# Performance work log

Hardware: AMD Instinct MI355X
Metric: run time of the kernel (lower is better)

Reference implementation:

```python
import jax, jax.numpy as jnp
import numpy as np

B, NN, S = 8, 511, 512          # graphs, nodes, seq (= nodes + graph token)
D, H, DH = 768, 12, 64          # hidden, heads, head dim
FFN, L = 3072, 6                # ffn size, layers
VOCAB = 512

def layer_norm(x, s, b, eps=1e-5):
    m = x.mean(-1, keepdims=True)
    v = ((x - m) ** 2).mean(-1, keepdims=True)
    return (x - m) / jnp.sqrt(v + eps) * s + b

def setup_inputs() -> dict:
    key = jax.random.key(0)
    ks = jax.random.split(key, 24)
    std = 0.02 / np.sqrt(L)
    inp = {}
    inp['attn_bias'] = jax.random.normal(ks[0], (B, S, S), jnp.float32) * 0.1
    inp['spatial_pos'] = jax.random.normal(ks[1], (B, NN, NN, 1), jnp.float32)
    inp['x'] = jax.random.randint(ks[2], (B, NN, 1), 0, VOCAB)
    node_emb = jax.random.normal(ks[3], (VOCAB, D), jnp.float32) * 0.02
    inp['node_emb'] = node_emb.at[0].set(0.0)  # padding_idx=0
    inp['graph_token'] = jax.random.normal(ks[4], (1, D), jnp.float32) * 0.02
    inp['virt_dist'] = jax.random.normal(ks[5], (1, H), jnp.float32) * 0.02
    inp['sp_w1'] = jax.random.normal(ks[6], (1, 128), jnp.float32) * std
    inp['sp_b1'] = jnp.zeros((128,), jnp.float32)
    inp['sp_w2'] = jax.random.normal(ks[7], (128, H), jnp.float32) * std
    inp['sp_b2'] = jnp.zeros((H,), jnp.float32)
    inp['ln1_s'] = jnp.ones((L, D), jnp.float32)
    inp['ln1_b'] = jnp.zeros((L, D), jnp.float32)
    inp['wq'] = jax.random.normal(ks[8], (L, D, D), jnp.float32) * std
    inp['bq'] = jnp.zeros((L, D), jnp.float32)
    inp['wk'] = jax.random.normal(ks[9], (L, D, D), jnp.float32) * std
    inp['bk'] = jnp.zeros((L, D), jnp.float32)
    inp['wv'] = jax.random.normal(ks[10], (L, D, D), jnp.float32) * std
    inp['bv'] = jnp.zeros((L, D), jnp.float32)
    inp['wo'] = jax.random.normal(ks[11], (L, D, D), jnp.float32) * std
    inp['bo'] = jnp.zeros((L, D), jnp.float32)
    inp['ln2_s'] = jnp.ones((L, D), jnp.float32)
    inp['ln2_b'] = jnp.zeros((L, D), jnp.float32)
    inp['fw1'] = jax.random.normal(ks[12], (L, D, FFN), jnp.float32) * std
    inp['fb1'] = jnp.zeros((L, FFN), jnp.float32)
    inp['fw2'] = jax.random.normal(ks[13], (L, FFN, D), jnp.float32) * std
    inp['fb2'] = jnp.zeros((L, D), jnp.float32)
    inp['fln_s'] = jnp.ones((D,), jnp.float32)
    inp['fln_b'] = jnp.zeros((D,), jnp.float32)
    return inp

def reference(attn_bias, spatial_pos, x, node_emb, graph_token, virt_dist,
              sp_w1, sp_b1, sp_w2, sp_b2,
              ln1_s, ln1_b, wq, bq, wk, bk, wv, bv, wo, bo,
              ln2_s, ln2_b, fw1, fb1, fw2, fb2, fln_s, fln_b):
    scale = DH ** -0.5
    # node features: embedding lookup summed over per-node feature indices
    h = node_emb[x].sum(axis=-2)                                   # [B, NN, D]
    h = jnp.concatenate([jnp.broadcast_to(graph_token[None], (B, 1, D)), h], axis=1)  # [B, S, D]
    # structural bias: spatial-pos MLP -> per-head bias on node block
    sp_bias = (spatial_pos @ sp_w1 + sp_b1) @ sp_w2 + sp_b2        # [B, NN, NN, H]
    sp_bias = sp_bias.transpose(0, 3, 1, 2)                         # [B, H, NN, NN]
    # original adds attn_bias twice (clone-repeat, then + attn_bias.unsqueeze(1))
    bias = jnp.broadcast_to((2.0 * attn_bias)[:, None], (B, H, S, S))
    t = virt_dist.reshape(1, H, 1)
    bias = bias.at[:, :, 1:, 1:].add(sp_bias)
    bias = bias.at[:, :, 1:, 0].add(t)
    bias = bias.at[:, :, 0, :].add(t)
    for l in range(L):
        y = layer_norm(h, ln1_s[l], ln1_b[l])
        q = (y @ wq[l] + bq[l]).reshape(B, S, H, DH) * scale
        k = (y @ wk[l] + bk[l]).reshape(B, S, H, DH)
        v = (y @ wv[l] + bv[l]).reshape(B, S, H, DH)
        scores = jnp.einsum('bihd,bjhd->bhij', q, k) + bias
        att = jax.nn.softmax(scores, axis=-1)
        o = jnp.einsum('bhij,bjhd->bihd', att, v).reshape(B, S, D)
        h = h + (o @ wo[l] + bo[l])
        y = layer_norm(h, ln2_s[l], ln2_b[l])
        h = h + (jax.nn.gelu(y @ fw1[l] + fb1[l], approximate=False) @ fw2[l] + fb2[l])
    return layer_norm(h, fln_s, fln_b)
```

## Files before the change

### kernel.cpp

```cpp
#include <hip/hip_runtime.h>
#include <cstdint>
#include <cstddef>


typedef __attribute__((ext_vector_type(8))) short bf16x8;
typedef __attribute__((ext_vector_type(4))) short bf16x4;
typedef __attribute__((ext_vector_type(4))) float f32x4;
typedef __attribute__((ext_vector_type(4))) unsigned int u32x4;

static constexpr int D    = 768;
static constexpr int H    = 12;
static constexpr int S    = 512;
static constexpr int NN   = 511;
static constexpr int B    = 8;
static constexpr int FFN  = 3072;
static constexpr int ROWS = B * S;

__device__ __forceinline__ short f2b(float x) {
    union { float f; uint32_t u; } c; c.f = x;
    uint32_t r = (c.u + 0x7fffu + ((c.u >> 16) & 1u)) >> 16;
    return (short)(uint16_t)r;
}
__device__ __forceinline__ float b2f_lo(uint32_t u) {
    union { uint32_t u; float f; } c; c.u = u << 16; return c.f;
}
__device__ __forceinline__ float b2f_hi(uint32_t u) {
    union { uint32_t u; float f; } c; c.u = u & 0xffff0000u; return c.f;
}
__device__ __forceinline__ float gelu_f(float x) {
    return 0.5f * x * (1.0f + erff(x * 0.7071067811865476f));
}
__device__ __forceinline__ void gload16(const void* g, void* l) {
    __builtin_amdgcn_global_load_lds(
        (const __attribute__((address_space(1))) void*)g,
        (__attribute__((address_space(3))) void*)l, 16, 0, 0);
}

#if __has_builtin(__builtin_amdgcn_mfma_f32_16x16x16bf16_1k)
__device__ __forceinline__ f32x4 mfma16(bf16x4 a, bf16x4 b, f32x4 c) {
    return __builtin_amdgcn_mfma_f32_16x16x16bf16_1k(a, b, c, 0, 0, 0);
}
__device__ __forceinline__ void mfma16_fence(f32x4* o) { (void)o; }
#else
__device__ __forceinline__ f32x4 mfma16(bf16x4 a, bf16x4 b, f32x4 c) {
    asm volatile("s_nop 1\n\tv_mfma_f32_16x16x16_bf16 %0, %1, %2, %0"
                 : "+v"(c) : "v"(a), "v"(b));
    return c;
}
__device__ __forceinline__ void mfma16_fence(f32x4* o) {
    asm volatile("s_nop 7\n\ts_nop 7"
                 : "+v"(o[0]), "+v"(o[1]), "+v"(o[2]), "+v"(o[3]));
}
#endif

__global__ __launch_bounds__(256) void embed_kernel(
    const int* __restrict__ x, const float* __restrict__ emb,
    const float* __restrict__ gtok, float* __restrict__ h)
{
    int row = blockIdx.x;
    int b = row >> 9, s = row & (S - 1);
    const float* src = (s == 0) ? gtok : (emb + (size_t)x[b * NN + (s - 1)] * D);
    float* dst = h + (size_t)row * D;
    int t = threadIdx.x;
    dst[t]       = src[t];
    dst[t + 256] = src[t + 256];
    dst[t + 512] = src[t + 512];
}

__global__ void ac_kernel(const float* __restrict__ w1, const float* __restrict__ b1,
                          const float* __restrict__ w2, const float* __restrict__ b2,
                          float* __restrict__ ac)
{
    int h = threadIdx.x;
    if (h < H) {
        float a = 0.f, c = 0.f;
        for (int k = 0; k < 128; ++k) { a += w1[k] * w2[k * H + h]; c += b1[k] * w2[k * H + h]; }
        ac[h] = a; ac[16 + h] = c + b2[h];
    }
}

__global__ __launch_bounds__(256) void bias_pack_kernel(
    const float* __restrict__ ab, const float* __restrict__ sp,
    uint32_t* __restrict__ pb)
{
    int row = blockIdx.x;
    int b = row >> 9, i = row & 511;
    const float* abr = ab + (size_t)row * S;
    const float* spr = sp + ((size_t)b * NN + (i - 1)) * NN;
    uint32_t* out = pb + (size_t)row * S;
    #pragma unroll
    for (int jt = 0; jt < 2; ++jt) {
        int j = jt * 256 + threadIdx.x;
        float a2 = 2.f * abr[j];
        float spv = (i > 0 && j > 0) ? spr[j - 1] : 0.f;
        out[j] = (uint32_t)(uint16_t)f2b(a2) | ((uint32_t)(uint16_t)f2b(spv) << 16);
    }
}

__global__ __launch_bounds__(256) void wcvt_kernel(
    const float* __restrict__ wq, const float* __restrict__ wk,
    const float* __restrict__ wv, const float* __restrict__ wo,
    const float* __restrict__ f1, const float* __restrict__ f2,
    short* __restrict__ wqkvT, short* __restrict__ woT,
    short* __restrict__ f1T, short* __restrict__ f2T)
{
    int t = blockIdx.x;
    const float* in; short* out; int R, C, tr, tc;
    if (t < 432) {
        int which = t / 144, tt = t - which * 144;
        in = (which == 0) ? wq : ((which == 1) ? wk : wv);
        out = wqkvT + (size_t)which * 768 * 768;
        R = 768; C = 768; tr = tt / 12; tc = tt % 12;
    } else if (t < 576) {
        int tt = t - 432; in = wo; out = woT; R = 768; C = 768; tr = tt / 12; tc = tt % 12;
    } else if (t < 1152) {
        int tt = t - 576; in = f1; out = f1T; R = 768; C = 3072; tr = tt / 48; tc = tt % 48;
    } else {
        int tt = t - 1152; in = f2; out = f2T; R = 3072; C = 768; tr = tt / 12; tc = tt % 12;
    }
    int r0 = tr * 64, c0 = tc * 64;
    __shared__ short tile[64][65];
    int tid = threadIdx.x;
    #pragma unroll
    for (int i = 0; i < 16; ++i) {
        int e = i * 256 + tid; int r = e >> 6, c = e & 63;
        tile[r][c] = f2b(in[(size_t)(r0 + r) * C + c0 + c]);
    }
    __syncthreads();
    #pragma unroll
    for (int i = 0; i < 16; ++i) {
        int e = i * 256 + tid; int c = e >> 6, r = e & 63;
        out[(size_t)(c0 + c) * R + r0 + r] = tile[r][c];
    }
}

__global__ __launch_bounds__(256) void ln_kernel(
    const float* __restrict__ in, const float* __restrict__ sc,
    const float* __restrict__ bi, float* __restrict__ outF,
    short* __restrict__ outB)
{
    int row = blockIdx.x, t = threadIdx.x;
    const float* x = in + (size_t)row * D;
    float e0 = x[t], e1 = x[t + 256], e2 = x[t + 512];
    float s  = e0 + e1 + e2;
    float sq = e0 * e0 + e1 * e1 + e2 * e2;
    #pragma unroll
    for (int off = 1; off < 64; off <<= 1) { s += __shfl_xor(s, off); sq += __shfl_xor(sq, off); }
    __shared__ float red[8];
    int w = t >> 6, lane = t & 63;
    if (lane == 0) { red[w] = s; red[4 + w] = sq; }
    __syncthreads();
    s  = red[0] + red[1] + red[2] + red[3];
    sq = red[4] + red[5] + red[6] + red[7];
    float m   = s * (1.f / D);
    float inv = rsqrtf(sq * (1.f / D) - m * m + 1e-5f);
    float v0 = (e0 - m) * inv * sc[t]       + bi[t];
    float v1 = (e1 - m) * inv * sc[t + 256] + bi[t + 256];
    float v2 = (e2 - m) * inv * sc[t + 512] + bi[t + 512];
    if (outB) {
        short* o = outB + (size_t)row * D;
        o[t] = f2b(v0); o[t + 256] = f2b(v1); o[t + 512] = f2b(v2);
    } else {
        float* o = outF + (size_t)row * D;
        o[t] = v0; o[t + 256] = v1; o[t + 512] = v2;
    }
}

template<int BM>
__global__ __launch_bounds__(256) void gemm2(
    const short* __restrict__ A, const short* __restrict__ Wt,
    const float* __restrict__ Bb0, const float* __restrict__ Bb1, const float* __restrict__ Bb2,
    float* __restrict__ outF, const float* __restrict__ resid,
    short* __restrict__ outB,
    int K, int nper, int gx, float alpha0, int mode)
{
    constexpr int MR = BM / 32;
    __shared__ __align__(16) short As[2][BM * 32];
    __shared__ __align__(16) short Bs[2][128 * 32];
    int tid  = threadIdx.x;
    int lane = tid & 63;
    int w    = tid >> 6;

    int nwg = gridDim.x;
    int bid = blockIdx.x;
    int sid = (bid & 7) * (nwg >> 3) + (bid >> 3);
    int row0 = (sid % gx) * BM;
    int n0   = (sid / gx) * 128;

    int which = n0 / nper;
    int ncol0 = n0 - which * nper;
    const float* Bv = (which == 0) ? Bb0 : ((which == 1) ? Bb1 : Bb2);
    float alpha = (which == 0) ? alpha0 : 1.0f;

    int wr = (w >> 1) * (BM / 2);
    int wc = (w & 1) * 64;
    int fr = lane & 15;
    int q4 = lane >> 4;

    f32x4 acc[MR][4] = {};

    auto stageA = [&](int buf, int k0) {
        #pragma unroll
        for (int ii = 0; ii < BM / 64; ++ii) {
            int U = ii * 256 + tid;
            int r = U >> 2;
            int ch = (U & 3) ^ ((r >> 1) & 3);
            gload16(A + (size_t)(row0 + r) * K + k0 + ch * 8,
                    (char*)&As[buf][0] + ((size_t)ii * 256 + w * 64) * 16);
        }
    };
    auto stageB = [&](int buf, int k0) {
        #pragma unroll
        for (int ii = 0; ii < 2; ++ii) {
            int U = ii * 256 + tid;
            int r = U >> 2;
            int ch = (U & 3) ^ ((r >> 1) & 3);
            gload16(Wt + (size_t)(n0 + r) * K + k0 + ch * 8,
                    (char*)&Bs[buf][0] + ((size_t)ii * 256 + w * 64) * 16);
        }
    };
    auto compute = [&](int buf) {
        bf16x8 af[MR], bfr[4];
        #pragma unroll
        for (int m = 0; m < MR; ++m) {
            int r = wr + m * 16 + fr;
            af[m] = *(const bf16x8*)((const char*)&As[buf][0]
                    + (size_t)r * 64 + ((q4 ^ ((r >> 1) & 3)) * 16));
        }
        #pragma unroll
        for (int n = 0; n < 4; ++n) {
            int r = wc + n * 16 + fr;
            bfr[n] = *(const bf16x8*)((const char*)&Bs[buf][0]
                    + (size_t)r * 64 + ((q4 ^ ((r >> 1) & 3)) * 16));
        }
        #pragma unroll
        for (int m = 0; m < MR; ++m)
            #pragma unroll
            for (int n = 0; n < 4; ++n)
                acc[m][n] = __builtin_amdgcn_mfma_f32_16x16x32_bf16(af[m], bfr[n], acc[m][n], 0, 0, 0);
    };

    int nt = K >> 5;
    stageA(0, 0); stageB(0, 0);
    __syncthreads();
    int cur = 0;
    for (int t = 1; t < nt; ++t) {
        stageA(cur ^ 1, t * 32);
        stageB(cur ^ 1, t * 32);
        compute(cur);
        __syncthreads();
        cur ^= 1;
    }
    compute(cur);

    int rr = q4 * 4;
    if (mode == 1) {
        short* base = outB + (size_t)which * ROWS * D;
        #pragma unroll
        for (int m = 0; m < MR; ++m) {
            int rowb = row0 + wr + m * 16 + rr;
            int b2 = rowb >> 9, s0 = rowb & 511;
            #pragma unroll
            for (int n = 0; n < 4; ++n) {
                int col = ncol0 + wc + n * 16 + fr;
                int h2 = col >> 6, d2 = col & 63;
                float bv = Bv[col];
                if (which == 2) {
                    bf16x4 pk;
                    #pragma unroll
                    for (int ri = 0; ri < 4; ++ri) pk[ri] = f2b(acc[m][n][ri] + bv);
                    *(bf16x4*)&base[(((size_t)b2 * H + h2) * 64 + d2) * 512 + s0] = pk;
                } else {
                    #pragma unroll
                    for (int ri = 0; ri < 4; ++ri)
                        base[(((size_t)b2 * H + h2) * 512 + (s0 + ri)) * 64 + d2] =
                            f2b((acc[m][n][ri] + bv) * alpha);
                }
            }
        }
        return;
    }

    #pragma unroll
    for (int m = 0; m < MR; ++m) {
        #pragma unroll
        for (int n = 0; n < 4; ++n) {
            int col  = ncol0 + wc + n * 16 + fr;
            float bv = Bv[col];
            #pragma unroll
            for (int ri = 0; ri < 4; ++ri) {
                int row = row0 + wr + m * 16 + rr + ri;
                size_t idx = (size_t)row * nper + col;
                float val = acc[m][n][ri] + bv;
                if (mode == 2) {
                    outB[idx] = f2b(gelu_f(val));
                } else {
                    outF[idx] = val + resid[idx];
                }
            }
        }
    }
}

__global__ __launch_bounds__(256) void attn_kernel(
    const short* __restrict__ qb, const short* __restrict__ kbuf,
    const short* __restrict__ vtb,
    const uint32_t* __restrict__ pb,
    const float* __restrict__ vd, const float* __restrict__ ac,
    short* __restrict__ o)
{
    __shared__ __align__(16) short Ks[2][128 * 64];
    __shared__ __align__(16) short Vs[2][64 * 128];
    int tid = threadIdx.x, lane = tid & 63, w = tid >> 6;
    int bid = blockIdx.x;
    int b    = bid & 7;
    int qblk = (bid >> 3) & 7;
    int hh   = bid >> 6;
    int fr = lane & 15, g16 = lane >> 4;
    int kb8 = g16 * 8, rr = g16 * 4;
    int i0 = qblk * 64 + w * 16;
    int i  = i0 + fr;

    const short* qp = qb   + ((size_t)(b * H + hh) * S) * 64;
    const short* kp = kbuf + ((size_t)(b * H + hh) * S) * 64;
    const short* vp = vtb  + ((size_t)(b * H + hh) * 64) * S;

    bf16x8 aq0 = *(const bf16x8*)&qp[(i0 + fr) * 64 + kb8];
    bf16x8 aq1 = *(const bf16x8*)&qp[(i0 + fr) * 64 + 32 + kb8];

    float Ah = ac[hh], Ch = ac[16 + hh], th = vd[hh];
    const uint32_t* pbb = pb + (size_t)b * S * S + (size_t)i * S;

    auto stageK = [&](int buf, int j0) {
        #pragma unroll
        for (int ii = 0; ii < 4; ++ii) {
            int U = ii * 256 + tid;
            int r = U >> 3;
            int ch = (U & 7) ^ (r & 7);
            gload16(kp + (size_t)(j0 + r) * 64 + ch * 8,
                    (char*)&Ks[buf][0] + ((size_t)ii * 256 + w * 64) * 16);
        }
    };
    auto stageV = [&](int buf, int j0) {
        #pragma unroll
        for (int ii = 0; ii < 4; ++ii) {
            int U = ii * 256 + tid;
            int d = U >> 4;
            int s8 = (2 * (U & 15)) ^ (d & 14);
            gload16(vp + (size_t)d * S + j0 + s8 * 4,
                    (char*)&Vs[buf][0] + ((size_t)ii * 256 + w * 64) * 16);
        }
    };

    float m_run = -3.0e38f, l_run = 0.f;
    f32x4 oacc[4] = {};

    stageK(0, 0);
    stageV(0, 0);
    __syncthreads();
    int buf = 0;
    #pragma unroll 1
    for (int t = 0; t < 4; ++t) {
        if (t < 3) { stageK(buf ^ 1, (t + 1) * 128); stageV(buf ^ 1, (t + 1) * 128); }
        f32x4 s[8];
        #pragma unroll
        for (int jt = 0; jt < 8; ++jt) {
            int jb = t * 8 + jt;
            u32x4 u = *(const u32x4*)&pbb[jb * 16 + rr];
            f32x4 c;
            #pragma unroll
            for (int ri = 0; ri < 4; ++ri) {
                int j = jb * 16 + rr + ri;
                float bias = b2f_lo(u[ri]);
                if (i > 0 && j > 0) bias += b2f_hi(u[ri]) * Ah + Ch;
                if (i == 0 || j == 0) bias += th;
                c[ri] = bias;
            }
            int r = jt * 16 + fr;
            const char* krow = (const char*)&Ks[buf][0] + r * 128;
            bf16x8 kf0 = *(const bf16x8*)(krow + ((g16 ^ (r & 7)) * 16));
            bf16x8 kf1 = *(const bf16x8*)(krow + (((g16 + 4) ^ (r & 7)) * 16));
            c = __builtin_amdgcn_mfma_f32_16x16x32_bf16(kf0, aq0, c, 0, 0, 0);
            s[jt] = __builtin_amdgcn_mfma_f32_16x16x32_bf16(kf1, aq1, c, 0, 0, 0);
        }
        float tm = s[0][0];
        #pragma unroll
        for (int jt = 0; jt < 8; ++jt)
            #pragma unroll
            for (int ri = 0; ri < 4; ++ri) tm = fmaxf(tm, s[jt][ri]);
        tm = fmaxf(tm, __shfl_xor(tm, 16));
        tm = fmaxf(tm, __shfl_xor(tm, 32));
        float mnew = fmaxf(m_run, tm);
        float scale = __expf(m_run - mnew);
        l_run *= scale;
        #pragma unroll
        for (int ri = 0; ri < 4; ++ri) {
            float scr = __shfl(scale, rr + ri);
            #pragma unroll
            for (int dt = 0; dt < 4; ++dt) oacc[dt][ri] *= scr;
        }
        #pragma unroll
        for (int jt = 0; jt < 8; ++jt)
            #pragma unroll
            for (int ri = 0; ri < 4; ++ri) {
                float p = __expf(s[jt][ri] - mnew);
                s[jt][ri] = p;
                l_run += p;
            }
        #pragma unroll
        for (int jt = 0; jt < 8; ++jt) {
            bf16x4 pa;
            #pragma unroll
            for (int ri = 0; ri < 4; ++ri) pa[ri] = f2b(s[jt][ri]);
            #pragma unroll
            for (int dt = 0; dt < 4; ++dt) {
                int d = dt * 16 + fr;
                const char* vrow = (const char*)&Vs[buf][0] + d * 256;
                bf16x4 vb = *(const bf16x4*)(vrow + (((jt * 4 + g16) ^ (d & 14)) * 8));
                oacc[dt] = mfma16(pa, vb, oacc[dt]);
            }
        }
        m_run = mnew;
        __syncthreads();
        buf ^= 1;
    }
    mfma16_fence(oacc);

    l_run += __shfl_xor(l_run, 16);
    l_run += __shfl_xor(l_run, 32);
    float invl = 1.f / l_run;
    #pragma unroll
    for (int ri = 0; ri < 4; ++ri) {
        float ivr = __shfl(invl, rr + ri);
        #pragma unroll
        for (int dt = 0; dt < 4; ++dt)
            o[((size_t)(b * S + i0 + rr + ri) * H + hh) * 64 + dt * 16 + fr] =
                f2b(oacc[dt][ri] * ivr);
    }
}

extern "C" void kernel_launch(void* const* d_in, const int* in_sizes, int n_in,
                              void* d_out, int out_size, void* d_ws, size_t ws_size,
                              hipStream_t stream)
{
    const float* attn_bias   = (const float*)d_in[0];
    const float* spatial_pos = (const float*)d_in[1];
    const int*   xx          = (const int*)d_in[2];
    const float* node_emb    = (const float*)d_in[3];
    const float* graph_token = (const float*)d_in[4];
    const float* virt_dist   = (const float*)d_in[5];
    const float* sp_w1 = (const float*)d_in[6];
    const float* sp_b1 = (const float*)d_in[7];
    const float* sp_w2 = (const float*)d_in[8];
    const float* sp_b2 = (const float*)d_in[9];
    const float* ln1_s = (const float*)d_in[10];
    const float* ln1_b = (const float*)d_in[11];
    const float* wq = (const float*)d_in[12];
    const float* bq = (const float*)d_in[13];
    const float* wk = (const float*)d_in[14];
    const float* bk = (const float*)d_in[15];
    const float* wv = (const float*)d_in[16];
    const float* bv = (const float*)d_in[17];
    const float* wo = (const float*)d_in[18];
    const float* bo = (const float*)d_in[19];
    const float* ln2_s = (const float*)d_in[20];
    const float* ln2_b = (const float*)d_in[21];
    const float* fw1 = (const float*)d_in[22];
    const float* fb1 = (const float*)d_in[23];
    const float* fw2 = (const float*)d_in[24];
    const float* fb2 = (const float*)d_in[25];
    const float* fln_s = (const float*)d_in[26];
    const float* fln_b = (const float*)d_in[27];

    float* wsf = (float*)d_ws;
    const size_t SZ = (size_t)ROWS * D;
    float* h   = wsf;
    float* acb = wsf + SZ;
    short* s16 = (short*)(wsf + SZ + 64);
    short* yob = s16;
    short* g16b = s16 + SZ;
    short* bfq = g16b + (size_t)ROWS * FFN;
    short* wqkvT = bfq + 3 * SZ;
    short* woT   = wqkvT + 2304 * 768;
    short* f1T   = woT + 768 * 768;
    short* f2T   = f1T + (size_t)3072 * 768;
    uint32_t* pbias = (uint32_t*)(f2T + (size_t)768 * 3072);

    embed_kernel<<<ROWS, 256, 0, stream>>>(xx, node_emb, graph_token, h);
    ac_kernel<<<1, 64, 0, stream>>>(sp_w1, sp_b1, sp_w2, sp_b2, acb);
    bias_pack_kernel<<<ROWS, 256, 0, stream>>>(attn_bias, spatial_pos, pbias);

    for (int l = 0; l < 6; ++l) {
        wcvt_kernel<<<1728, 256, 0, stream>>>(
            wq + (size_t)l * D * D, wk + (size_t)l * D * D, wv + (size_t)l * D * D,
            wo + (size_t)l * D * D, fw1 + (size_t)l * D * FFN, fw2 + (size_t)l * FFN * D,
            wqkvT, woT, f1T, f2T);
        ln_kernel<<<ROWS, 256, 0, stream>>>(h, ln1_s + l * D, ln1_b + l * D, nullptr, yob);
        gemm2<128><<<576, 256, 0, stream>>>(
            yob, wqkvT, bq + l * D, bk + l * D, bv + l * D,
            nullptr, nullptr, bfq, D, D, 32, 0.125f, 1);
        attn_kernel<<<B * H * 8, 256, 0, stream>>>(
            bfq, bfq + SZ, bfq + 2 * SZ, pbias, virt_dist, acb, yob);
        gemm2<64><<<384, 256, 0, stream>>>(
            yob, woT, bo + l * D, nullptr, nullptr,
            h, h, nullptr, D, D, 64, 1.0f, 0);
        ln_kernel<<<ROWS, 256, 0, stream>>>(h, ln2_s + l * D, ln2_b + l * D, nullptr, yob);
        gemm2<128><<<768, 256, 0, stream>>>(
            yob, f1T, fb1 + l * FFN, nullptr, nullptr,
            nullptr, nullptr, g16b, D, FFN, 32, 1.0f, 2);
        gemm2<64><<<384, 256, 0, stream>>>(
            g16b, f2T, fb2 + l * D, nullptr, nullptr,
            h, h, nullptr, FFN, D, 64, 1.0f, 0);
    }
    ln_kernel<<<ROWS, 256, 0, stream>>>(h, fln_s, fln_b, (float*)d_out, nullptr);
}
```

Baseline: 1.247 ms.

## Split-K the FFN down-projection GEMM into four partials with a reduce kernel

The FFN2 GEMM (K=3072) now runs as a 4-way split-K, launching 1536 workgroups instead of 384 so more of the GPU's compute units are busy. Each split writes fp32 partial sums to a workspace buffer. A new reduce kernel then adds the partials, the bias and the residual into h. The cost is extra global traffic: four fp32 partial tensors of 4096x768 written and read back, plus one more kernel launch per layer.

```diff
diff --git a/kernel.cpp b/kernel.cpp
--- a/kernel.cpp
+++ b/kernel.cpp
@@ -166,13 +166,27 @@
     }
 }
 
+__global__ __launch_bounds__(256) void ffn2_reduce_kernel(
+    const float* __restrict__ pt, const float* __restrict__ fb2,
+    float* __restrict__ h)
+{
+    const size_t SZ = (size_t)ROWS * D;
+    int row = blockIdx.x, t = threadIdx.x;
+    #pragma unroll
+    for (int c = 0; c < 3; ++c) {
+        int col = t + c * 256;
+        size_t idx = (size_t)row * D + col;
+        h[idx] += fb2[col] + pt[idx] + pt[SZ + idx] + pt[2 * SZ + idx] + pt[3 * SZ + idx];
+    }
+}
+
 template<int BM>
 __global__ __launch_bounds__(256) void gemm2(
     const short* __restrict__ A, const short* __restrict__ Wt,
     const float* __restrict__ Bb0, const float* __restrict__ Bb1, const float* __restrict__ Bb2,
     float* __restrict__ outF, const float* __restrict__ resid,
     short* __restrict__ outB,
-    int K, int nper, int gx, float alpha0, int mode)
+    int K, int Kst, int nper, int gx, int nsplit, float alpha0, int mode)
 {
     constexpr int MR = BM / 32;
     __shared__ __align__(16) short As[2][BM * 32];
@@ -184,8 +198,14 @@
     int nwg = gridDim.x;
     int bid = blockIdx.x;
     int sid = (bid & 7) * (nwg >> 3) + (bid >> 3);
-    int row0 = (sid % gx) * BM;
-    int n0   = (sid / gx) * 128;
+    int per = nwg / nsplit;
+    int sp  = sid / per;
+    int rem = sid - sp * per;
+    int row0 = (rem % gx) * BM;
+    int n0   = (rem / gx) * 128;
+    A  += (size_t)sp * K;
+    Wt += (size_t)sp * K;
+    float* outFp = outF + (mode == 3 ? (size_t)sp * ROWS * nper : 0);
 
     int which = n0 / nper;
     int ncol0 = n0 - which * nper;
@@ -205,7 +225,7 @@
             int U = ii * 256 + tid;
             int r = U >> 2;
             int ch = (U & 3) ^ ((r >> 1) & 3);
-            gload16(A + (size_t)(row0 + r) * K + k0 + ch * 8,
+            gload16(A + (size_t)(row0 + r) * Kst + k0 + ch * 8,
                     (char*)&As[buf][0] + ((size_t)ii * 256 + w * 64) * 16);
         }
     };
@@ -215,7 +235,7 @@
             int U = ii * 256 + tid;
             int r = U >> 2;
             int ch = (U & 3) ^ ((r >> 1) & 3);
-            gload16(Wt + (size_t)(n0 + r) * K + k0 + ch * 8,
+            gload16(Wt + (size_t)(n0 + r) * Kst + k0 + ch * 8,
                     (char*)&Bs[buf][0] + ((size_t)ii * 256 + w * 64) * 16);
         }
     };
@@ -254,6 +274,20 @@
     compute(cur);
 
     int rr = q4 * 4;
+    if (mode == 3) {
+        #pragma unroll
+        for (int m = 0; m < MR; ++m)
+            #pragma unroll
+            for (int n = 0; n < 4; ++n) {
+                int col = ncol0 + wc + n * 16 + fr;
+                #pragma unroll
+                for (int ri = 0; ri < 4; ++ri) {
+                    int row = row0 + wr + m * 16 + rr + ri;
+                    outFp[(size_t)row * nper + col] = acc[m][n][ri];
+                }
+            }
+        return;
+    }
     if (mode == 1) {
         short* base = outB + (size_t)which * ROWS * D;
         #pragma unroll
@@ -485,6 +519,7 @@
     short* f1T   = woT + 768 * 768;
     short* f2T   = f1T + (size_t)3072 * 768;
     uint32_t* pbias = (uint32_t*)(f2T + (size_t)768 * 3072);
+    float* ptb = (float*)(pbias + (size_t)B * S * S);
 
     embed_kernel<<<ROWS, 256, 0, stream>>>(xx, node_emb, graph_token, h);
     ac_kernel<<<1, 64, 0, stream>>>(sp_w1, sp_b1, sp_w2, sp_b2, acb);
@@ -498,19 +533,20 @@
         ln_kernel<<<ROWS, 256, 0, stream>>>(h, ln1_s + l * D, ln1_b + l * D, nullptr, yob);
         gemm2<128><<<576, 256, 0, stream>>>(
             yob, wqkvT, bq + l * D, bk + l * D, bv + l * D,
-            nullptr, nullptr, bfq, D, D, 32, 0.125f, 1);
+            nullptr, nullptr, bfq, D, D, D, 32, 1, 0.125f, 1);
         attn_kernel<<<B * H * 8, 256, 0, stream>>>(
             bfq, bfq + SZ, bfq + 2 * SZ, pbias, virt_dist, acb, yob);
         gemm2<64><<<384, 256, 0, stream>>>(
             yob, woT, bo + l * D, nullptr, nullptr,
-            h, h, nullptr, D, D, 64, 1.0f, 0);
+            h, h, nullptr, D, D, D, 64, 1, 1.0f, 0);
         ln_kernel<<<ROWS, 256, 0, stream>>>(h, ln2_s + l * D, ln2_b + l * D, nullptr, yob);
         gemm2<128><<<768, 256, 0, stream>>>(
             yob, f1T, fb1 + l * FFN, nullptr, nullptr,
-            nullptr, nullptr, g16b, D, FFN, 32, 1.0f, 2);
-        gemm2<64><<<384, 256, 0, stream>>>(
-            g16b, f2T, fb2 + l * D, nullptr, nullptr,
-            h, h, nullptr, FFN, D, 64, 1.0f, 0);
+            nullptr, nullptr, g16b, D, D, FFN, 32, 1, 1.0f, 2);
+        gemm2<64><<<1536, 256, 0, stream>>>(
+            g16b, f2T, nullptr, nullptr, nullptr,
+            ptb, nullptr, nullptr, 768, FFN, D, 64, 4, 1.0f, 3);
+        ffn2_reduce_kernel<<<ROWS, 256, 0, stream>>>(ptb, fb2 + l * D, h);
     }
     ln_kernel<<<ROWS, 256, 0, stream>>>(h, fln_s, fln_b, (float*)d_out, nullptr);
 }
```

Measured after the change: 1.429 ms. +14.6%, slower.
